# Kernel optimization log

Measured on AMD Instinct MI355X. Metric: run time of the kernel, lower is better.

## Reference

```python
import jax, jax.numpy as jnp
from jax import lax
import numpy as np

NUM_POINTS = 2048  # init_kwargs: num_points
BIG = 1e10


def setup_inputs() -> dict:
    key = jax.random.key(0)
    points = jax.random.normal(key, (16, 3, 32768), dtype=jnp.float32)
    return {"points": points}


def furthest_point_sampling(xyz, m):
    """xyz: [B, N, 3]. Returns indices [B, m] (int32), first index = 0 (CUDA FPS convention)."""
    B, N, _ = xyz.shape

    def step(carry, _):
        dist, last_idx = carry                                   # [B,N], [B]
        last_pt = jnp.take_along_axis(xyz, last_idx[:, None, None], axis=1)  # [B,1,3]
        d = jnp.sum((xyz - last_pt) ** 2, axis=-1)               # [B,N]
        dist = jnp.minimum(dist, d)
        nxt = jnp.argmax(dist, axis=1).astype(jnp.int32)         # [B]
        return (dist, nxt), last_idx                             # emit current selection

    init = (jnp.full((B, N), BIG, dtype=xyz.dtype), jnp.zeros((B,), jnp.int32))
    _, idxs = lax.scan(step, init, None, length=m)               # [m, B]
    return idxs.T                                                # [B, m]


def fps_gather_by_index(points, idx):
    """points: [B, C, N]; idx: [B, m] -> [B, C, m]."""
    return jnp.take_along_axis(points, idx[:, None, :], axis=2)


def reference(points):
    xyz = jnp.transpose(points, (0, 2, 1))          # [B, N, 3]
    ind = furthest_point_sampling(xyz, NUM_POINTS)  # [B, M]
    return fps_gather_by_index(points, ind)         # [B, 3, M]
```

## Files before the change

### kernel.cpp

```cpp
#include <hip/hip_runtime.h>

#define FPS_N 32768
#define FPS_M 2048
#define FPS_B 16
#define BLK_PER_B 8
#define FPS_T 576
#define SCT 512
#define PTS (FPS_N / BLK_PER_B)
#define PPT (PTS / SCT)
#define KPUB 4
#define RING 128
#define WSTRIDE 960

typedef unsigned long long ull;

#define DPP_MAX_STEP(ctrl, rmask)                                              \
    {                                                                          \
        unsigned plo = (unsigned)__builtin_amdgcn_update_dpp(                  \
            (int)lo, (int)lo, (ctrl), (rmask), 0xf, false);                    \
        unsigned phi = (unsigned)__builtin_amdgcn_update_dpp(                  \
            (int)hi, (int)hi, (ctrl), (rmask), 0xf, false);                    \
        if (phi > hi || (phi == hi && plo > lo)) { hi = phi; lo = plo; }       \
    }

__device__ __forceinline__ ull wave_max_u64(ull v) {
    unsigned lo = (unsigned)v, hi = (unsigned)(v >> 32);
    DPP_MAX_STEP(0x111, 0xf)
    DPP_MAX_STEP(0x112, 0xf)
    DPP_MAX_STEP(0x114, 0xf)
    DPP_MAX_STEP(0x118, 0xf)
    DPP_MAX_STEP(0x142, 0xa)
    DPP_MAX_STEP(0x143, 0xc)
    unsigned blo = (unsigned)__builtin_amdgcn_readlane((int)lo, 63);
    unsigned bhi = (unsigned)__builtin_amdgcn_readlane((int)hi, 63);
    return ((ull)bhi << 32) | blo;
}

__device__ __forceinline__ unsigned wave_max_bits(unsigned v) {
    int m = (int)v;
#define DPP_IMAX_STEP(ctrl)                                                    \
    {                                                                          \
        int p = __builtin_amdgcn_update_dpp((int)m, (int)m, (ctrl), 0xf, 0xf,  \
                                            false);                            \
        m = p > m ? p : m;                                                     \
    }
    DPP_IMAX_STEP(0x111)
    DPP_IMAX_STEP(0x112)
    DPP_IMAX_STEP(0x114)
    DPP_IMAX_STEP(0x118)
    int r0 = __builtin_amdgcn_readlane(m, 15);
    int r1 = __builtin_amdgcn_readlane(m, 31);
    int r2 = __builtin_amdgcn_readlane(m, 47);
    int r3 = __builtin_amdgcn_readlane(m, 63);
    int a = r0 > r1 ? r0 : r1;
    int bq = r2 > r3 ? r2 : r3;
    return (unsigned)(a > bq ? a : bq);
}

__device__ __forceinline__ unsigned wave_min_u32(unsigned v) {
    unsigned m = v;
#define DPP_UMIN_STEP(ctrl, rmask)                                             \
    {                                                                          \
        unsigned p = (unsigned)__builtin_amdgcn_update_dpp(                    \
            (int)m, (int)m, (ctrl), (rmask), 0xf, false);                      \
        if (p < m) m = p;                                                      \
    }
    DPP_UMIN_STEP(0x111, 0xf)
    DPP_UMIN_STEP(0x112, 0xf)
    DPP_UMIN_STEP(0x114, 0xf)
    DPP_UMIN_STEP(0x118, 0xf)
    DPP_UMIN_STEP(0x142, 0xa)
    DPP_UMIN_STEP(0x143, 0xc)
    return (unsigned)__builtin_amdgcn_readlane((int)m, 63);
}

__device__ __forceinline__ float readlane_f(float v, int l) {
    return __uint_as_float(
        (unsigned)__builtin_amdgcn_readlane((int)__float_as_uint(v), l));
}

__device__ __forceinline__ void store_mirror_sc0(ull* p, ull w) {
    asm volatile("global_store_dwordx2 %0, %1, off sc0"
                 :: "v"((ull)(uintptr_t)p), "v"(w) : "memory");
}

__global__ __launch_bounds__(FPS_T)
__attribute__((amdgpu_waves_per_eu(1)))
void fps_kernel(const float* __restrict__ pts, float* __restrict__ out,
                ull* __restrict__ ws) {
#pragma clang fp contract(off)
    __shared__ float srx[RING], sry[RING], srz[RING];
    __shared__ unsigned rtag[RING];
    __shared__ unsigned etot;

    const int blk = blockIdx.x;
    const int b = blk & 15;
    const int j = blk >> 4;
    const int tid = threadIdx.x;
    const int lane = tid & 63;
    const float* __restrict__ X = pts + (size_t)b * 3 * FPS_N;
    const float* __restrict__ Y = X + FPS_N;
    const float* __restrict__ Z = Y + FPS_N;
    const int off = j * PTS;
    float* __restrict__ outb = out + (size_t)b * 3 * FPS_M;
    ull* __restrict__ wsb = ws + (size_t)b * WSTRIDE;
    ull* __restrict__ mir = wsb + 640;

    for (int q = tid; q < RING; q += FPS_T) rtag[q] = 0;
    if (tid == 0) etot = 0;
    __syncthreads();

    const float p0x = X[0], p0y = Y[0], p0z = Z[0];

    if (tid < 64) {
        if (j == 0 && lane == 0) {
            outb[0] = p0x; outb[FPS_M] = p0y; outb[2 * FPS_M] = p0z;
        }
        const ull ma0 = (ull)(uintptr_t)(mir + 0 * 64 + lane);
        const ull ma1 = (ull)(uintptr_t)(mir + 1 * 64 + lane);
        const ull ma2 = (ull)(uintptr_t)(mir + 2 * 64 + lane);
        const ull ma3 = (ull)(uintptr_t)(mir + 3 * 64 + lane);
        const ull mac = (ull)(uintptr_t)(mir + 256 + lane);
        int last = 0;
        for (unsigned e = 1; last < FPS_M - 1; ++e) {
            ull* const grp = wsb + (e & 1) * 320;
            ull cv[KPUB];
            float ccx[KPUB], ccy[KPUB], ccz[KPUB];
#pragma unroll
            for (int c = 0; c < KPUB; ++c) {
                cv[c] = 0; ccx[c] = 0.0f; ccy[c] = 0.0f; ccz[c] = 0.0f;
            }
            unsigned kcm = 0;
            bool kw = false;
            ull cw = 0;
            for (int it = 0; it < (1 << 25); ++it) {
                ull q0, q1, q2, q3, q4;
                asm volatile(
                    "global_load_dwordx2 %0, %5, off sc0\n\t"
                    "global_load_dwordx2 %1, %6, off sc0\n\t"
                    "global_load_dwordx2 %2, %7, off sc0\n\t"
                    "global_load_dwordx2 %3, %8, off sc0\n\t"
                    "global_load_dwordx2 %4, %9, off sc0\n\t"
                    "s_waitcnt vmcnt(0)"
                    : "=&v"(q0), "=&v"(q1), "=&v"(q2), "=&v"(q3), "=&v"(q4)
                    : "v"(ma0), "v"(ma1), "v"(ma2), "v"(ma3), "v"(mac)
                    : "memory");
                ull pv[KPUB + 1] = {q0, q1, q2, q3, q4};
#pragma unroll
                for (int c = 0; c < KPUB; ++c) {
                    if (!(kcm & (1u << c)) &&
                        (unsigned)(pv[c] & 0xFFFull) == e) {
                        cv[c] = pv[c];
                        kcm |= 1u << c;
                        const int g = 32767 - (int)((pv[c] >> 17) & 0x7FFFull);
                        ccx[c] = X[g];
                        ccy[c] = Y[g];
                        ccz[c] = Z[g];
                    }
                }
                if (!kw && (unsigned)(pv[KPUB] & 0xFFFull) == e) {
                    cw = pv[KPUB]; kw = true;
                }
                bool done = __all((kcm == ((1u << KPUB) - 1)) && kw);
                if (!done) {
                    ull av[KPUB + 1];
#pragma unroll
                    for (int c = 0; c < KPUB; ++c)
                        av[c] = (kcm & (1u << c))
                                    ? 0
                                    : __hip_atomic_load(grp + c * 64 + lane,
                                                        __ATOMIC_RELAXED,
                                                        __HIP_MEMORY_SCOPE_AGENT);
                    av[KPUB] = kw ? 0
                                  : __hip_atomic_load(grp + 256 + lane,
                                                      __ATOMIC_RELAXED,
                                                      __HIP_MEMORY_SCOPE_AGENT);
#pragma unroll
                    for (int c = 0; c < KPUB; ++c) {
                        if (!(kcm & (1u << c)) &&
                            (unsigned)(av[c] & 0xFFFull) == e) {
                            cv[c] = av[c];
                            kcm |= 1u << c;
                            const int g =
                                32767 - (int)((av[c] >> 17) & 0x7FFFull);
                            ccx[c] = X[g];
                            ccy[c] = Y[g];
                            ccz[c] = Z[g];
                        }
                    }
                    if (!kw && (unsigned)(av[KPUB] & 0xFFFull) == e) {
                        cw = av[KPUB]; kw = true;
                    }
                    done = __all((kcm == ((1u << KPUB) - 1)) && kw);
                }
                if (done) break;
                __builtin_amdgcn_s_sleep(1);
            }
            const ull vcutg = wave_max_u64(cw);
            int posted = 0;
            while (last < FPS_M - 1 && posted < RING) {
                ull m = cv[0];
#pragma unroll
                for (int c = 1; c < KPUB; ++c)
                    if (cv[c] > m) m = cv[c];
                const unsigned mhi = (unsigned)(m >> 32);
                const unsigned Whi = wave_max_bits(mhi);
                const ull tb = __ballot(mhi == Whi);
                ull W;
                if (__popcll(tb) == 1) {
                    const int wl0 = (int)(__ffsll((long long)tb) - 1);
                    const unsigned wlo = (unsigned)__builtin_amdgcn_readlane(
                        (int)(unsigned)(m & 0xFFFFFFFFull), wl0);
                    W = ((ull)Whi << 32) | wlo;
                } else {
                    W = wave_max_u64(m);
                }
                if (W <= vcutg) break;
                bool own = false;
                float sx = 0.0f, sy = 0.0f, sz = 0.0f;
#pragma unroll
                for (int c = 0; c < KPUB; ++c) {
                    const bool h = (cv[c] == W);
                    own |= h;
                    sx = h ? ccx[c] : sx;
                    sy = h ? ccy[c] : sy;
                    sz = h ? ccz[c] : sz;
                    cv[c] = h ? 0 : cv[c];
                }
                const ull mk = __ballot(own);
                const int wl = __ffsll((long long)mk) - 1;
                const float wx = readlane_f(sx, wl);
                const float wy = readlane_f(sy, wl);
                const float wz = readlane_f(sz, wl);
#pragma unroll
                for (int c = 0; c < KPUB; ++c) {
                    float dx = ccx[c] - wx, dy = ccy[c] - wy, dz = ccz[c] - wz;
                    float d = (dx * dx + dy * dy) + dz * dz;
                    float df = __uint_as_float((unsigned)(cv[c] >> 32));
                    float nd = d < df ? d : df;
                    cv[c] = ((ull)__float_as_uint(nd) << 32)
                          | (cv[c] & 0xFFFFFFFFull);
                }
                ++last; ++posted;
                const int slot = last & (RING - 1);
                if (lane == 0) {
                    srx[slot] = wx; sry[slot] = wy; srz[slot] = wz;
                    __hip_atomic_store(&rtag[slot], (unsigned)last,
                                       __ATOMIC_RELEASE,
                                       __HIP_MEMORY_SCOPE_WORKGROUP);
                }
            }
            if (lane == 0)
                __hip_atomic_store(&etot, (e << 16) | (unsigned)last,
                                   __ATOMIC_RELAXED, __HIP_MEMORY_SCOPE_WORKGROUP);
        }
    } else {
        const int st = tid - 64;
        const int w = (tid >> 6) - 1;
        const int wid = j * 8 + w;
        float cx[PPT], cy[PPT], cz[PPT], dist[PPT];
#pragma unroll
        for (int k = 0; k < PPT; ++k) {
            const int g = off + k * SCT + st;
            cx[k] = X[g]; cy[k] = Y[g]; cz[k] = Z[g];
            float dx = cx[k] - p0x, dy = cy[k] - p0y, dz = cz[k] - p0z;
            dist[k] = (dx * dx + dy * dy) + dz * dz;
        }
        const int goff = off + st;
        unsigned applied = 0;
        for (unsigned e = 1;; ++e) {
            ull* const grp = wsb + (e & 1) * 320;
            float fd[PPT];
#pragma unroll
            for (int k = 0; k < PPT; ++k) fd[k] = dist[k];
            for (int r = 0; r < KPUB + 1; ++r) {
                float m = fd[0];
#pragma unroll
                for (int k = 1; k < PPT; ++k) m = fmaxf(m, fd[k]);
                const unsigned Wb = wave_max_bits(__float_as_uint(m));
                unsigned mg = 0xFFFFFFFFu;
#pragma unroll
                for (int k = PPT - 1; k >= 0; --k)
                    if (__float_as_uint(fd[k]) == Wb)
                        mg = (unsigned)(goff + k * SCT);
                const ull mk = __ballot(mg != 0xFFFFFFFFu);
                unsigned gw;
                if (__popcll(mk) == 1) {
                    gw = (unsigned)__builtin_amdgcn_readlane(
                        (int)mg, (int)(__ffsll((long long)mk) - 1));
                } else {
                    gw = wave_min_u32(mg);
                }
                const ull word = ((ull)Wb << 32)
                               | ((ull)(32767u - gw) << 17) | (ull)e;
                if (r < KPUB) {
#pragma unroll
                    for (int k = 0; k < PPT; ++k)
                        if ((unsigned)(goff + k * SCT) == gw)
                            fd[k] = -1.0f;
                    if (lane == r) {
                        store_mirror_sc0(mir + r * 64 + wid, word);
                        __hip_atomic_store(grp + r * 64 + wid, word,
                                           __ATOMIC_RELAXED,
                                           __HIP_MEMORY_SCOPE_AGENT);
                    }
                } else {
                    if (lane == KPUB) {
                        store_mirror_sc0(mir + 256 + wid, word);
                        __hip_atomic_store(grp + 256 + wid, word,
                                           __ATOMIC_RELAXED,
                                           __HIP_MEMORY_SCOPE_AGENT);
                    }
                }
            }
            unsigned last_row = 0;
            bool have = false;
            for (;;) {
                bool did = false;
                if (!have) {
                    unsigned u = __hip_atomic_load(&etot, __ATOMIC_RELAXED,
                                                   __HIP_MEMORY_SCOPE_WORKGROUP);
                    if ((u >> 16) == e) { last_row = u & 0xFFFFu; have = true; did = true; }
                }
                const unsigned want = applied + 1;
                if (!have || want <= last_row) {
                    const int slot = (int)(want & (RING - 1));
                    if (__hip_atomic_load(&rtag[slot], __ATOMIC_ACQUIRE,
                                          __HIP_MEMORY_SCOPE_WORKGROUP) == want) {
                        const float wx = srx[slot], wy = sry[slot], wz = srz[slot];
#pragma unroll
                        for (int k = 0; k < PPT; ++k) {
                            float dx = cx[k] - wx, dy = cy[k] - wy, dz = cz[k] - wz;
                            float d = (dx * dx + dy * dy) + dz * dz;
                            dist[k] = d < dist[k] ? d : dist[k];
                        }
                        if (j == 0 && w == 0 && lane < 3) {
                            float cvv = lane == 0 ? wx : (lane == 1 ? wy : wz);
                            outb[(size_t)lane * FPS_M + want] = cvv;
                        }
                        applied = want;
                        did = true;
                    }
                }
                if (have && applied == last_row) break;
                if (!did) __builtin_amdgcn_s_sleep(1);
            }
            if (last_row >= FPS_M - 1) break;
        }
    }
}

extern "C" void kernel_launch(void* const* d_in, const int* in_sizes, int n_in,
                              void* d_out, int out_size, void* d_ws, size_t ws_size,
                              hipStream_t stream) {
    const float* pts = (const float*)d_in[0];
    float* out = (float*)d_out;
    ull* ws = (ull*)d_ws;
    void* args[] = { (void*)&pts, (void*)&out, (void*)&ws };
    hipLaunchCooperativeKernel((const void*)fps_kernel,
                               dim3(FPS_B * BLK_PER_B), dim3(FPS_T),
                               args, 0, stream);
}
```

Measured before the change: 1.212 ms.

## Extract top-2 candidates per wave reduction in FPS candidate publishing

```diff
diff --git a/kernel.cpp b/kernel.cpp
--- a/kernel.cpp
+++ b/kernel.cpp
@@ -57,6 +57,47 @@
     return (unsigned)(a > bq ? a : bq);
 }
 
+__device__ __forceinline__ void wave_top2_bits(unsigned v1, unsigned v2,
+                                               unsigned& o1, unsigned& o2) {
+    int m1 = (int)v1, m2 = (int)v2;
+#define DPP_PAIR_STEP(ctrl)                                                    \
+    {                                                                          \
+        int p1 = __builtin_amdgcn_update_dpp(m1, m1, (ctrl), 0xf, 0xf, false); \
+        int p2 = __builtin_amdgcn_update_dpp(m2, m2, (ctrl), 0xf, 0xf, false); \
+        int lo_ = m1 < p1 ? m1 : p1;                                           \
+        int hi_ = m1 > p1 ? m1 : p1;                                           \
+        int s2_ = m2 > p2 ? m2 : p2;                                           \
+        m1 = hi_;                                                              \
+        m2 = lo_ > s2_ ? lo_ : s2_;                                            \
+    }
+    DPP_PAIR_STEP(0x111)
+    DPP_PAIR_STEP(0x112)
+    DPP_PAIR_STEP(0x114)
+    DPP_PAIR_STEP(0x118)
+    int a1 = __builtin_amdgcn_readlane(m1, 15);
+    int a2 = __builtin_amdgcn_readlane(m2, 15);
+    int b1 = __builtin_amdgcn_readlane(m1, 31);
+    int b2 = __builtin_amdgcn_readlane(m2, 31);
+    int c1 = __builtin_amdgcn_readlane(m1, 47);
+    int c2 = __builtin_amdgcn_readlane(m2, 47);
+    int d1 = __builtin_amdgcn_readlane(m1, 63);
+    int d2 = __builtin_amdgcn_readlane(m2, 63);
+    int ab1 = a1 > b1 ? a1 : b1;
+    int abl = a1 < b1 ? a1 : b1;
+    int abs_ = a2 > b2 ? a2 : b2;
+    int ab2 = abl > abs_ ? abl : abs_;
+    int cd1 = c1 > d1 ? c1 : d1;
+    int cdl = c1 < d1 ? c1 : d1;
+    int cds_ = c2 > d2 ? c2 : d2;
+    int cd2 = cdl > cds_ ? cdl : cds_;
+    int f1 = ab1 > cd1 ? ab1 : cd1;
+    int fl = ab1 < cd1 ? ab1 : cd1;
+    int fs_ = ab2 > cd2 ? ab2 : cd2;
+    int f2 = fl > fs_ ? fl : fs_;
+    o1 = (unsigned)f1;
+    o2 = (unsigned)f2;
+}
+
 __device__ __forceinline__ unsigned wave_min_u32(unsigned v) {
     unsigned m = v;
 #define DPP_UMIN_STEP(ctrl, rmask)                                             \
@@ -79,9 +120,31 @@
         (unsigned)__builtin_amdgcn_readlane((int)__float_as_uint(v), l));
 }
 
-__device__ __forceinline__ void store_mirror_sc0(ull* p, ull w) {
-    asm volatile("global_store_dwordx2 %0, %1, off sc0"
-                 :: "v"((ull)(uintptr_t)p), "v"(w) : "memory");
+__device__ __forceinline__ unsigned resolve_idx(const float (&fd)[PPT],
+                                                int goff, unsigned Wb) {
+    unsigned mg = 0xFFFFFFFFu;
+#pragma unroll
+    for (int k = PPT - 1; k >= 0; --k)
+        if (__float_as_uint(fd[k]) == Wb) mg = (unsigned)(goff + k * SCT);
+    const ull mk = __ballot(mg != 0xFFFFFFFFu);
+    if (__popcll(mk) == 1)
+        return (unsigned)__builtin_amdgcn_readlane(
+            (int)mg, (int)(__ffsll((long long)mk) - 1));
+    return wave_min_u32(mg);
+}
+
+__device__ __forceinline__ void mask_idx(float (&fd)[PPT], int goff,
+                                         unsigned gw) {
+#pragma unroll
+    for (int k = 0; k < PPT; ++k)
+        if ((unsigned)(goff + k * SCT) == gw) fd[k] = -1.0f;
+}
+
+__device__ __forceinline__ void publish2(ull* mir, ull* grp, int slot, ull w) {
+    __hip_atomic_store(mir + slot, w, __ATOMIC_RELAXED,
+                       __HIP_MEMORY_SCOPE_WORKGROUP);
+    __hip_atomic_store(grp + slot, w, __ATOMIC_RELAXED,
+                       __HIP_MEMORY_SCOPE_AGENT);
 }
 
 __global__ __launch_bounds__(FPS_T)
@@ -273,45 +336,71 @@
             float fd[PPT];
 #pragma unroll
             for (int k = 0; k < PPT; ++k) fd[k] = dist[k];
-            for (int r = 0; r < KPUB + 1; ++r) {
-                float m = fd[0];
-#pragma unroll
-                for (int k = 1; k < PPT; ++k) m = fmaxf(m, fd[k]);
+            int rank = 0;
+            bool cut_done = false;
+            while (rank < KPUB) {
+                int v0 = (int)__float_as_uint(fd[0]);
+                int v1 = (int)__float_as_uint(fd[1]);
+                int v2 = (int)__float_as_uint(fd[2]);
+                int v3 = (int)__float_as_uint(fd[3]);
+                int v4 = (int)__float_as_uint(fd[4]);
+                int v5 = (int)__float_as_uint(fd[5]);
+                int v6 = (int)__float_as_uint(fd[6]);
+                int v7 = (int)__float_as_uint(fd[7]);
+                int h0 = v0 > v1 ? v0 : v1, l0 = v0 > v1 ? v1 : v0;
+                int h1 = v2 > v3 ? v2 : v3, l1 = v2 > v3 ? v3 : v2;
+                int h2 = v4 > v5 ? v4 : v5, l2 = v4 > v5 ? v5 : v4;
+                int h3 = v6 > v7 ? v6 : v7, l3 = v6 > v7 ? v7 : v6;
+                int A1 = h0 > h1 ? h0 : h1;
+                int Al = h0 < h1 ? h0 : h1;
+                int As = l0 > l1 ? l0 : l1;
+                int A2 = Al > As ? Al : As;
+                int B1 = h2 > h3 ? h2 : h3;
+                int Bl = h2 < h3 ? h2 : h3;
+                int Bs = l2 > l3 ? l2 : l3;
+                int B2 = Bl > Bs ? Bl : Bs;
+                int M1 = A1 > B1 ? A1 : B1;
+                int Ml = A1 < B1 ? A1 : B1;
+                int Ms = A2 > B2 ? A2 : B2;
+                int M2 = Ml > Ms ? Ml : Ms;
+                unsigned W1b, W2b;
+                wave_top2_bits((unsigned)M1, (unsigned)M2, W1b, W2b);
+                if (W1b != W2b) {
+                    const unsigned g1 = resolve_idx(fd, goff, W1b);
+                    const unsigned g2 = resolve_idx(fd, goff, W2b);
+                    const ull w1 = ((ull)W1b << 32)
+                                 | ((ull)(32767u - g1) << 17) | (ull)e;
+                    const ull w2 = ((ull)W2b << 32)
+                                 | ((ull)(32767u - g2) << 17) | (ull)e;
+                    if (lane == rank) publish2(mir, grp, rank * 64 + wid, w1);
+                    if (rank + 1 < KPUB) {
+                        if (lane == rank + 1)
+                            publish2(mir, grp, (rank + 1) * 64 + wid, w2);
+                        mask_idx(fd, goff, g1);
+                        mask_idx(fd, goff, g2);
+                        rank += 2;
+                    } else {
+                        if (lane == KPUB) publish2(mir, grp, 256 + wid, w2);
+                        rank += 2;
+                        cut_done = true;
+                    }
+                } else {
+                    const unsigned g1 = resolve_idx(fd, goff, W1b);
+                    const ull w1 = ((ull)W1b << 32)
+                                 | ((ull)(32767u - g1) << 17) | (ull)e;
+                    if (lane == rank) publish2(mir, grp, rank * 64 + wid, w1);
+                    mask_idx(fd, goff, g1);
+                    ++rank;
+                }
+            }
+            if (!cut_done) {
+                float m = fmaxf(fmaxf(fmaxf(fd[0], fd[1]), fmaxf(fd[2], fd[3])),
+                                fmaxf(fmaxf(fd[4], fd[5]), fmaxf(fd[6], fd[7])));
                 const unsigned Wb = wave_max_bits(__float_as_uint(m));
-                unsigned mg = 0xFFFFFFFFu;
-#pragma unroll
-                for (int k = PPT - 1; k >= 0; --k)
-                    if (__float_as_uint(fd[k]) == Wb)
-                        mg = (unsigned)(goff + k * SCT);
-                const ull mk = __ballot(mg != 0xFFFFFFFFu);
-                unsigned gw;
-                if (__popcll(mk) == 1) {
-                    gw = (unsigned)__builtin_amdgcn_readlane(
-                        (int)mg, (int)(__ffsll((long long)mk) - 1));
-                } else {
-                    gw = wave_min_u32(mg);
-                }
+                const unsigned gw = resolve_idx(fd, goff, Wb);
                 const ull word = ((ull)Wb << 32)
                                | ((ull)(32767u - gw) << 17) | (ull)e;
-                if (r < KPUB) {
-#pragma unroll
-                    for (int k = 0; k < PPT; ++k)
-                        if ((unsigned)(goff + k * SCT) == gw)
-                            fd[k] = -1.0f;
-                    if (lane == r) {
-                        store_mirror_sc0(mir + r * 64 + wid, word);
-                        __hip_atomic_store(grp + r * 64 + wid, word,
-                                           __ATOMIC_RELAXED,
-                                           __HIP_MEMORY_SCOPE_AGENT);
-                    }
-                } else {
-                    if (lane == KPUB) {
-                        store_mirror_sc0(mir + 256 + wid, word);
-                        __hip_atomic_store(grp + 256 + wid, word,
-                                           __ATOMIC_RELAXED,
-                                           __HIP_MEMORY_SCOPE_AGENT);
-                    }
-                }
+                if (lane == KPUB) publish2(mir, grp, 256 + wid, word);
             }
             unsigned last_row = 0;
             bool have = false;
```

New measurement: 1.199 ms. Within noise of the previous version (-1.1%).
